# Performance work log

Hardware: AMD Instinct MI355X
Metric: run time of the kernel (lower is better)

The kernel has to match this reference:

```python
import jax, jax.numpy as jnp
import numpy as np

N_NODES = 20000
N_EDGES = 640000
CHANNELS = 128
EDGE_ATTR_DIM = 1


def setup_inputs() -> dict:
    key = jax.random.key(0)
    ks = jax.random.split(key, 10)
    C, E, N = CHANNELS, N_EDGES, N_NODES
    x_a = jax.random.normal(ks[0], (N, C), dtype=jnp.float32)
    edge_index = jax.random.randint(ks[1], (2, E), 0, N, dtype=jnp.int64)
    edge_attr = jax.random.uniform(ks[2], (E, EDGE_ATTR_DIM), dtype=jnp.float32)
    # Linear params (stored as [in, out]); scaled like torch default init
    g_in = 2 * C + EDGE_ATTR_DIM
    g_w = jax.random.uniform(ks[3], (g_in, C), jnp.float32, -1, 1) / np.sqrt(g_in)
    g_b = jax.random.uniform(ks[4], (C,), jnp.float32, -1, 1) / np.sqrt(g_in)
    f_w = jax.random.uniform(ks[5], (2 * C, C), jnp.float32, -1, 1) / np.sqrt(2 * C)
    f_b = jax.random.uniform(ks[6], (C,), jnp.float32, -1, 1) / np.sqrt(2 * C)
    cls_w = jax.random.uniform(ks[7], (C, 1), jnp.float32, -1, 1) / np.sqrt(C)
    cls_b = jax.random.uniform(ks[8], (1,), jnp.float32, -1, 1) / np.sqrt(C)
    return {"x_a": x_a, "edge_index": edge_index, "edge_attr": edge_attr,
            "g_w": g_w, "g_b": g_b, "f_w": f_w, "f_b": f_b,
            "cls_w": cls_w, "cls_b": cls_b}


def reference(x_a, edge_index, edge_attr, g_w, g_b, f_w, f_b, cls_w, cls_b):
    # PyG MessagePassing (flow source_to_target): x_j = x[src], x_i = x[dst]
    src = edge_index[0]
    dst = edge_index[1]
    N = x_a.shape[0]
    # message: g([x_i, x_j, e_ij])  -> [E, C]
    z_ij = jnp.concatenate([x_a[dst], x_a[src], edge_attr], axis=-1)
    msg = z_ij @ g_w + g_b
    # aggregate: scatter-mean over destination nodes (empty nodes -> 0)
    sums = jax.ops.segment_sum(msg, dst, num_segments=N)
    cnt = jax.ops.segment_sum(jnp.ones((dst.shape[0], 1), x_a.dtype), dst,
                              num_segments=N)
    aggr = sums / jnp.maximum(cnt, 1.0)
    # update: f([x, aggr])
    h = jnp.concatenate([x_a, aggr], axis=-1) @ f_w + f_b
    # classifier + sigmoid + threshold
    probs = jax.nn.sigmoid(h @ cls_w + cls_b)
    y = probs > 0.5
    return (y, probs)
```

## Files before the change

kernel.cpp:

```cpp
#include <hip/hip_runtime.h>
#include <math.h>

#define NNODES 20000
#define NEDGES 640000
#define C 128

#define NB 128
#define BT 1024

#define CNT_SHIFT 26
#define EDGE_BIAS (1 << 19)
#define SUM_MASK 0x03FFFFFFu

__global__ void __launch_bounds__(BT)
k_node(const float* __restrict__ x,
       const float* __restrict__ g_w, const float* __restrict__ g_b,
       const float* __restrict__ f_w, const float* __restrict__ f_b,
       const float* __restrict__ cls_w, const float* __restrict__ cls_b,
       float* __restrict__ xu, float* __restrict__ xp,
       float* __restrict__ r, float* __restrict__ scal)
{
    __shared__ float csh[C], vsh[C], ush[C], psh[C], qsh[C];
    __shared__ float red[BT];
    const int tid = threadIdx.x;

    {
        int pair = tid >> 2;
        int prt  = tid & 3;
        int k = pair & 127;
        int h = pair >> 7;

        if (tid < C) csh[tid] = cls_w[tid];
        __syncthreads();

        const float4* fw4 = (const float4*)f_w;
        const float4* gw4 = (const float4*)g_w;
        const float4* cs4 = (const float4*)csh;

        {
            const float4* row = fw4 + (size_t)(h * C + k) * (C / 4) + prt * 8;
            const float4* cc  = cs4 + prt * 8;
            float s = 0.f;
            #pragma unroll
            for (int j = 0; j < 8; ++j) {
                float4 a = row[j], c = cc[j];
                s += a.x * c.x + a.y * c.y + a.z * c.z + a.w * c.w;
            }
            red[tid] = s;
        }
        __syncthreads();
        if (prt == 0) {
            float tot = red[tid] + red[tid + 1] + red[tid + 2] + red[tid + 3];
            if (h == 0) ush[k] = tot; else vsh[k] = tot;
        }
        __syncthreads();

        const float4* vs4 = (const float4*)vsh;
        {
            const float4* row = gw4 + (size_t)(h * C + k) * (C / 4) + prt * 8;
            const float4* vv  = vs4 + prt * 8;
            float s = 0.f;
            #pragma unroll
            for (int j = 0; j < 8; ++j) {
                float4 a = row[j], c = vv[j];
                s += a.x * c.x + a.y * c.y + a.z * c.z + a.w * c.w;
            }
            red[tid] = s;
        }
        __syncthreads();
        if (prt == 0) {
            float tot = red[tid] + red[tid + 1] + red[tid + 2] + red[tid + 3];
            if (h == 0) psh[k] = tot; else qsh[k] = tot;
        }
        __syncthreads();

        if (tid < C) red[tid] = g_b[tid] * vsh[tid];
        __syncthreads();
        for (int s = 64; s > 0; s >>= 1) { if (tid < s) red[tid] += red[tid + s]; __syncthreads(); }
        if (tid == 0) scal[0] = red[0];
        __syncthreads();
        if (tid < C) red[tid] = g_w[256 * C + tid] * vsh[tid];
        __syncthreads();
        for (int s = 64; s > 0; s >>= 1) { if (tid < s) red[tid] += red[tid + s]; __syncthreads(); }
        if (tid == 0) scal[1] = red[0];
        __syncthreads();
        if (tid < C) red[tid] = f_b[tid] * csh[tid];
        __syncthreads();
        for (int s = 64; s > 0; s >>= 1) { if (tid < s) red[tid] += red[tid + s]; __syncthreads(); }
        if (tid == 0) scal[2] = red[0] + cls_b[0];
        __syncthreads();
    }

    {
        int w = tid >> 6, lane = tid & 63;
        int gwave = blockIdx.x * (BT / 64) + w;
        float2 uu = ((const float2*)ush)[lane];
        float2 pp = ((const float2*)psh)[lane];
        float2 qq = ((const float2*)qsh)[lane];

        for (int n = gwave; n < NNODES; n += 256 * (BT / 64)) {
            float2 xx = ((const float2*)(x + (size_t)n * C))[lane];
            float du = xx.x * uu.x + xx.y * uu.y;
            float dp = xx.x * pp.x + xx.y * pp.y;
            float dq = xx.x * qq.x + xx.y * qq.y;
            for (int off = 32; off > 0; off >>= 1) {
                du += __shfl_down(du, off);
                dp += __shfl_down(dp, off);
                dq += __shfl_down(dq, off);
            }
            if (lane == 0) { xu[n] = du; xp[n] = dp; r[n] = dq; }
        }
    }
}

__global__ void __launch_bounds__(BT)
k_edge(const int* __restrict__ ei, const float* __restrict__ attr,
       const float* __restrict__ r, const float* __restrict__ scal,
       unsigned int* __restrict__ part)
{
    __shared__ unsigned int lacc[NNODES];
    int tid = threadIdx.x;

    uint4* l4 = (uint4*)lacc;
    for (int i = tid; i < NNODES / 4; i += BT) l4[i] = make_uint4(0u, 0u, 0u, 0u);
    __syncthreads();

    float gev = scal[1];
    for (int e = blockIdx.x * BT + tid; e < NEDGES; e += NB * BT) {
        int s = ei[e];
        int d = ei[NEDGES + e];
        float t = r[s] + attr[e] * gev;
        int fix = __float2int_rn(t * 65536.0f);
        atomicAdd(&lacc[d], (1u << CNT_SHIFT) + (unsigned int)(fix + EDGE_BIAS));
    }
    __syncthreads();

    uint4* mp4 = (uint4*)(part + (size_t)blockIdx.x * NNODES);
    for (int i = tid; i < NNODES / 4; i += BT) mp4[i] = l4[i];
}

__global__ void __launch_bounds__(256)
k_final(const float* __restrict__ xu, const float* __restrict__ xp,
        const unsigned int* __restrict__ part,
        const float* __restrict__ scal, float* __restrict__ out)
{
    int t = threadIdx.x;
    int quad = t >> 2;
    int prt  = t & 3;
    int n = blockIdx.x * 64 + quad;

    int sumfix = 0, cnt = 0;
    if (n < NNODES) {
        const unsigned int* pb = part + (size_t)(prt * (NB / 4)) * NNODES + n;
        #pragma unroll
        for (int b = 0; b < NB / 4; ++b) {
            unsigned int v = pb[(size_t)b * NNODES];
            int c = (int)(v >> CNT_SHIFT);
            cnt += c;
            sumfix += (int)(v & SUM_MASK) - (c << 19);
        }
    }
    sumfix += __shfl_down(sumfix, 1);
    sumfix += __shfl_down(sumfix, 2);
    cnt    += __shfl_down(cnt, 1);
    cnt    += __shfl_down(cnt, 2);

    if (prt == 0 && n < NNODES) {
        float sacc = (float)sumfix * (1.0f / 65536.0f);
        float cmax = fmaxf((float)cnt, 1.0f);
        float cfac = (cnt > 0) ? 1.0f : 0.0f;
        float logit = xu[n] + cfac * (xp[n] + scal[0]) + sacc / cmax + scal[2];
        float pr = 1.0f / (1.0f + expf(-logit));
        out[n] = (pr > 0.5f) ? 1.0f : 0.0f;
        out[NNODES + n] = pr;
    }
}

extern "C" void kernel_launch(void* const* d_in, const int* in_sizes, int n_in,
                              void* d_out, int out_size, void* d_ws, size_t ws_size,
                              hipStream_t stream) {
    const float* x_a       = (const float*)d_in[0];
    const int*   ei        = (const int*)d_in[1];
    const float* edge_attr = (const float*)d_in[2];
    const float* g_w       = (const float*)d_in[3];
    const float* g_b       = (const float*)d_in[4];
    const float* f_w       = (const float*)d_in[5];
    const float* f_b       = (const float*)d_in[6];
    const float* cls_w     = (const float*)d_in[7];
    const float* cls_b     = (const float*)d_in[8];
    float* out = (float*)d_out;

    unsigned int* part = (unsigned int*)d_ws;
    float* xu   = (float*)d_ws + (size_t)NB * NNODES;
    float* xp   = xu + NNODES;
    float* r    = xp + NNODES;
    float* scal = r + NNODES;

    k_node<<<256, BT, 0, stream>>>(x_a, g_w, g_b, f_w, f_b, cls_w, cls_b,
                                   xu, xp, r, scal);

    k_edge<<<NB, BT, 0, stream>>>(ei, edge_attr, r, scal, part);

    k_final<<<(NNODES + 63) / 64, 256, 0, stream>>>(xu, xp, part, scal, out);
}
```

Measured before the change: 104.0 us.

## Replace per-block LDS partials with global 64-bit atomics and fused last-block finalize

Edge aggregation no longer builds per-block shared-memory histograms that are written to a partial buffer and reduced by a separate kernel. Each edge now does a packed 64-bit global atomicAdd (count in the high bits, fixed-point sum in the low bits) into a per-node accumulator that the node kernel zeroes. A ticket counter lets the last finishing block compute the sigmoid outputs, which removes the third launch and the large partial-buffer traffic. The cost is heavy global atomic contention across 640k edges and a serial finalize done by a single block over 20k nodes.

```diff
diff --git a/kernel.cpp b/kernel.cpp
--- a/kernel.cpp
+++ b/kernel.cpp
@@ -5,12 +5,14 @@
 #define NEDGES 640000
 #define C 128
 
-#define NB 128
+#define NB1 256
 #define BT 1024
 
-#define CNT_SHIFT 26
-#define EDGE_BIAS (1 << 19)
-#define SUM_MASK 0x03FFFFFFu
+#define NB2 320
+#define BT2 1024
+
+#define SUM_BITS 40
+#define FIX_BIAS (1 << 20)
 
 __global__ void __launch_bounds__(BT)
 k_node(const float* __restrict__ x,
@@ -18,11 +20,18 @@
        const float* __restrict__ f_w, const float* __restrict__ f_b,
        const float* __restrict__ cls_w, const float* __restrict__ cls_b,
        float* __restrict__ xu, float* __restrict__ xp,
-       float* __restrict__ r, float* __restrict__ scal)
+       float* __restrict__ r, float* __restrict__ scal,
+       unsigned long long* __restrict__ acc, unsigned int* __restrict__ done)
 {
     __shared__ float csh[C], vsh[C], ush[C], psh[C], qsh[C];
     __shared__ float red[BT];
     const int tid = threadIdx.x;
+
+    {
+        int i = blockIdx.x * BT + tid;
+        if (i < NNODES) acc[i] = 0ull;
+        if (blockIdx.x == 0 && tid == 0) *done = 0u;
+    }
 
     {
         int pair = tid >> 2;
@@ -98,7 +107,7 @@
         float2 pp = ((const float2*)psh)[lane];
         float2 qq = ((const float2*)qsh)[lane];
 
-        for (int n = gwave; n < NNODES; n += 256 * (BT / 64)) {
+        for (int n = gwave; n < NNODES; n += NB1 * (BT / 64)) {
             float2 xx = ((const float2*)(x + (size_t)n * C))[lane];
             float du = xx.x * uu.x + xx.y * uu.y;
             float dp = xx.x * pp.x + xx.y * pp.y;
@@ -113,63 +122,48 @@
     }
 }
 
-__global__ void __launch_bounds__(BT)
-k_edge(const int* __restrict__ ei, const float* __restrict__ attr,
-       const float* __restrict__ r, const float* __restrict__ scal,
-       unsigned int* __restrict__ part)
+__global__ void __launch_bounds__(BT2)
+k_edge_final(const int* __restrict__ ei, const float* __restrict__ attr,
+             const float* __restrict__ r, const float* __restrict__ scal,
+             const float* __restrict__ xu, const float* __restrict__ xp,
+             unsigned long long* __restrict__ acc,
+             unsigned int* __restrict__ done,
+             float* __restrict__ out)
 {
-    __shared__ unsigned int lacc[NNODES];
-    int tid = threadIdx.x;
+    __shared__ unsigned int ticket;
+    const int tid = threadIdx.x;
+    const float gev = scal[1];
 
-    uint4* l4 = (uint4*)lacc;
-    for (int i = tid; i < NNODES / 4; i += BT) l4[i] = make_uint4(0u, 0u, 0u, 0u);
-    __syncthreads();
-
-    float gev = scal[1];
-    for (int e = blockIdx.x * BT + tid; e < NEDGES; e += NB * BT) {
+    for (int e = blockIdx.x * BT2 + tid; e < NEDGES; e += NB2 * BT2) {
         int s = ei[e];
         int d = ei[NEDGES + e];
         float t = r[s] + attr[e] * gev;
         int fix = __float2int_rn(t * 65536.0f);
-        atomicAdd(&lacc[d], (1u << CNT_SHIFT) + (unsigned int)(fix + EDGE_BIAS));
+        unsigned long long add = (1ull << SUM_BITS)
+                               | (unsigned long long)(unsigned int)(fix + FIX_BIAS);
+        atomicAdd(&acc[d], add);
+    }
+
+    __syncthreads();
+    if (tid == 0) {
+        __threadfence();
+        ticket = atomicAdd(done, 1u);
     }
     __syncthreads();
+    if (ticket != NB2 - 1) return;
+    __threadfence();
 
-    uint4* mp4 = (uint4*)(part + (size_t)blockIdx.x * NNODES);
-    for (int i = tid; i < NNODES / 4; i += BT) mp4[i] = l4[i];
-}
-
-__global__ void __launch_bounds__(256)
-k_final(const float* __restrict__ xu, const float* __restrict__ xp,
-        const unsigned int* __restrict__ part,
-        const float* __restrict__ scal, float* __restrict__ out)
-{
-    int t = threadIdx.x;
-    int quad = t >> 2;
-    int prt  = t & 3;
-    int n = blockIdx.x * 64 + quad;
-
-    int sumfix = 0, cnt = 0;
-    if (n < NNODES) {
-        const unsigned int* pb = part + (size_t)(prt * (NB / 4)) * NNODES + n;
-        #pragma unroll
-        for (int b = 0; b < NB / 4; ++b) {
-            unsigned int v = pb[(size_t)b * NNODES];
-            int c = (int)(v >> CNT_SHIFT);
-            cnt += c;
-            sumfix += (int)(v & SUM_MASK) - (c << 19);
-        }
-    }
-    sumfix += __shfl_down(sumfix, 1);
-    sumfix += __shfl_down(sumfix, 2);
-    cnt    += __shfl_down(cnt, 1);
-    cnt    += __shfl_down(cnt, 2);
-
-    if (prt == 0 && n < NNODES) {
+    const float s0 = scal[0], s2 = scal[2];
+    for (int n = tid; n < NNODES; n += BT2) {
+        unsigned long long v = __hip_atomic_load(&acc[n], __ATOMIC_RELAXED,
+                                                 __HIP_MEMORY_SCOPE_AGENT);
+        unsigned int cnt = (unsigned int)(v >> SUM_BITS);
+        long long sumfix = (long long)(v & ((1ull << SUM_BITS) - 1))
+                         - ((long long)cnt << 20);
         float sacc = (float)sumfix * (1.0f / 65536.0f);
         float cmax = fmaxf((float)cnt, 1.0f);
         float cfac = (cnt > 0) ? 1.0f : 0.0f;
-        float logit = xu[n] + cfac * (xp[n] + scal[0]) + sacc / cmax + scal[2];
+        float logit = xu[n] + cfac * (xp[n] + s0) + sacc / cmax + s2;
         float pr = 1.0f / (1.0f + expf(-logit));
         out[n] = (pr > 0.5f) ? 1.0f : 0.0f;
         out[NNODES + n] = pr;
@@ -190,16 +184,16 @@
     const float* cls_b     = (const float*)d_in[8];
     float* out = (float*)d_out;
 
-    unsigned int* part = (unsigned int*)d_ws;
-    float* xu   = (float*)d_ws + (size_t)NB * NNODES;
+    unsigned long long* acc = (unsigned long long*)d_ws;
+    float* xu   = (float*)(acc + NNODES);
     float* xp   = xu + NNODES;
     float* r    = xp + NNODES;
     float* scal = r + NNODES;
+    unsigned int* done = (unsigned int*)(scal + 4);
 
-    k_node<<<256, BT, 0, stream>>>(x_a, g_w, g_b, f_w, f_b, cls_w, cls_b,
-                                   xu, xp, r, scal);
+    k_node<<<NB1, BT, 0, stream>>>(x_a, g_w, g_b, f_w, f_b, cls_w, cls_b,
+                                   xu, xp, r, scal, acc, done);
 
-    k_edge<<<NB, BT, 0, stream>>>(ei, edge_attr, r, scal, part);
-
-    k_final<<<(NNODES + 63) / 64, 256, 0, stream>>>(xu, xp, part, scal, out);
+    k_edge_final<<<NB2, BT2, 0, stream>>>(ei, edge_attr, r, scal, xu, xp,
+                                          acc, done, out);
 }
```

After: 139.9 us. +34.5%, slower.
